# Performance work log

Hardware: AMD Instinct MI355X
Metric: run time of the kernel (lower is better)

The kernel has to match this reference:

```python
import jax, jax.numpy as jnp
import numpy as np
from jax import lax

B, S, D, H = 32, 1024, 1024, 1024


def setup_inputs() -> dict:
    key = jax.random.key(0)
    k_x, k_wx, k_wh, k_b = jax.random.split(key, 4)
    x = jax.random.normal(k_x, (B, S, D), dtype=jnp.float32)
    # Vanilla RNN cell parameters: h' = tanh(x @ Wx + h @ Wh + b)
    Wx = jax.random.normal(k_wx, (D, H), dtype=jnp.float32) / np.sqrt(D)
    Wh = jax.random.normal(k_wh, (H, H), dtype=jnp.float32) / np.sqrt(H)
    b = jnp.zeros((H,), dtype=jnp.float32)
    # initial_hidden weight, zero-initialized as in the keras layer
    h0 = jnp.zeros((H,), dtype=jnp.float32)
    return {"x": x, "Wx": Wx, "Wh": Wh, "b": b, "h0": h0}


def reference(x, Wx, Wh, b, h0):
    # x: [B, S, D] -> scan over time (seq-major, like tf.scan on transposed input)
    batch = x.shape[0]
    h_init = jnp.tile(h0[None, :], (batch, 1))  # [B, H]

    def step(h, x_t):
        h_new = jnp.tanh(x_t @ Wx + h @ Wh + b)  # [B, H]
        return h_new, h_new

    x_sbd = jnp.transpose(x, (1, 0, 2))  # [S, B, D]
    _, out_sbh = lax.scan(step, h_init, x_sbd)
    return jnp.transpose(out_sbh, (1, 0, 2))  # [B, S, H]
```

## Files before the change

kernel.cpp:

```cpp
#include <hip/hip_runtime.h>
#include <hip/hip_bf16.h>


#define BB 32
#define SS 1024
#define DD 1024
#define HH 1024
#define NG 32
#define BG 8
#define WGN (NG * BG)

#define CFENCE() asm volatile("" ::: "memory")

typedef unsigned long long ull;

__global__ __launch_bounds__(256) void xw_gemm(const float* __restrict__ A,
                                               const float* __restrict__ W,
                                               const float* __restrict__ bias,
                                               float* __restrict__ C) {
    __shared__ float As[8][132];
    __shared__ float Bs[8][132];
    const int tid = threadIdx.x;
    const int n0 = blockIdx.x * 128;
    const int m0 = blockIdx.y * 128;
    const int tx = tid & 15;
    const int ty = tid >> 4;
    const int ar = tid >> 1;
    const int ak = (tid & 1) * 4;
    const int bk = tid >> 5;
    const int bn = (tid & 31) * 4;

    float acc[8][8];
#pragma unroll
    for (int i = 0; i < 8; ++i)
#pragma unroll
        for (int j = 0; j < 8; ++j) acc[i][j] = 0.f;

    for (int k0 = 0; k0 < DD; k0 += 8) {
        float4 av = *(const float4*)(A + (size_t)(m0 + ar) * DD + k0 + ak);
        float4 bv = *(const float4*)(W + (size_t)(k0 + bk) * HH + n0 + bn);
        __syncthreads();
        As[ak + 0][ar] = av.x;
        As[ak + 1][ar] = av.y;
        As[ak + 2][ar] = av.z;
        As[ak + 3][ar] = av.w;
        *(float4*)&Bs[bk][bn] = bv;
        __syncthreads();
#pragma unroll
        for (int k = 0; k < 8; ++k) {
            float4 a0 = *(const float4*)&As[k][ty * 4];
            float4 a1 = *(const float4*)&As[k][64 + ty * 4];
            float4 b0 = *(const float4*)&Bs[k][tx * 4];
            float4 b1 = *(const float4*)&Bs[k][64 + tx * 4];
            float ar_[8] = {a0.x, a0.y, a0.z, a0.w, a1.x, a1.y, a1.z, a1.w};
            float br_[8] = {b0.x, b0.y, b0.z, b0.w, b1.x, b1.y, b1.z, b1.w};
#pragma unroll
            for (int i = 0; i < 8; ++i)
#pragma unroll
                for (int j = 0; j < 8; ++j)
                    acc[i][j] = fmaf(ar_[i], br_[j], acc[i][j]);
        }
    }

    float4 bv0 = *(const float4*)(bias + n0 + tx * 4);
    float4 bv1 = *(const float4*)(bias + n0 + 64 + tx * 4);
#pragma unroll
    for (int i = 0; i < 8; ++i) {
        int m = m0 + ((i < 4) ? (ty * 4 + i) : (64 + ty * 4 + (i - 4)));
        float4 r0 = {acc[i][0] + bv0.x, acc[i][1] + bv0.y,
                     acc[i][2] + bv0.z, acc[i][3] + bv0.w};
        float4 r1 = {acc[i][4] + bv1.x, acc[i][5] + bv1.y,
                     acc[i][6] + bv1.z, acc[i][7] + bv1.w};
        *(float4*)(C + (size_t)m * HH + n0 + tx * 4) = r0;
        *(float4*)(C + (size_t)m * HH + n0 + 64 + tx * 4) = r1;
    }
}

__global__ __launch_bounds__(256) void transpose_wh(const float* __restrict__ in,
                                                    float* __restrict__ outT) {
    __shared__ float tile[32][33];
    const int tx = threadIdx.x & 31;
    const int ty = threadIdx.x >> 5;
    const int x0 = blockIdx.x * 32;
    const int y0 = blockIdx.y * 32;
    for (int r = ty; r < 32; r += 8)
        tile[r][tx] = in[(size_t)(y0 + r) * HH + x0 + tx];
    __syncthreads();
    for (int r = ty; r < 32; r += 8)
        outT[(size_t)(x0 + r) * HH + y0 + tx] = tile[tx][r];
}

#define FMA_HALF(HALF)                                                         \
    {                                                                          \
        const int kb = (HALF) * 512 + kq * 4;                                  \
        float4 h[4];                                                           \
        _Pragma("unroll") for (int b = 0; b < 4; ++b)                          \
            h[b] = *(const float4*)&hs[b][kb];                                 \
        _Pragma("unroll") for (int b = 0; b < 4; ++b)                          \
            _Pragma("unroll") for (int c = 0; c < 16; ++c)                     \
                a[b * 16 + c] += h[b].x * wreg[HALF][c].x +                    \
                                 h[b].y * wreg[HALF][c].y +                    \
                                 h[b].z * wreg[HALF][c].z +                    \
                                 h[b].w * wreg[HALF][c].w;                     \
    }

__global__ __launch_bounds__(256, 1) void rnn_persist(
    const float* __restrict__ Wh, const float* __restrict__ WhT,
    const float* __restrict__ h0, float* __restrict__ out,
    unsigned int* __restrict__ flags, float* __restrict__ hbuf) {
    __shared__ float hs[4][1024];
    __shared__ float red[4][64];
    __shared__ float hout[4][32];

    const int tid  = threadIdx.x;
    const int ng   = blockIdx.x & 31;
    const int bg   = blockIdx.x >> 5;
    const int n0   = ng * 32;
    const int b0   = bg * 4;
    const int lane = tid & 63;
    const int wv   = tid >> 6;
    const int ns   = tid >> 7;
    const int kq   = tid & 127;
    unsigned int* cnt = flags + bg * 64;

    float4 wreg[2][16];
    if (WhT) {
        const float* base = WhT + (size_t)(n0 + ns * 16) * HH + kq * 4;
#pragma unroll
        for (int c = 0; c < 16; ++c) {
            wreg[0][c] = *(const float4*)(base + (size_t)c * HH);
            wreg[1][c] = *(const float4*)(base + (size_t)c * HH + 512);
        }
    } else {
#pragma unroll
        for (int c = 0; c < 16; ++c) {
            float v[8];
            for (int j = 0; j < 4; ++j)
                v[j] = Wh[(size_t)(kq * 4 + j) * HH + n0 + ns * 16 + c];
            for (int j = 0; j < 4; ++j)
                v[4 + j] = Wh[(size_t)(512 + kq * 4 + j) * HH + n0 + ns * 16 + c];
            wreg[0][c] = {v[0], v[1], v[2], v[3]};
            wreg[1][c] = {v[4], v[5], v[6], v[7]};
        }
    }

    size_t xp_base = 0;
    int eb = 0, ec = 0;
    if (tid < 128) {
        int l   = tid & 63;
        int idx = (int)(__brev((unsigned)l) >> 26);
        eb = idx >> 4;
        ec = (tid >> 6) * 16 + (idx & 15);
        xp_base = ((size_t)(b0 + eb) * SS) * HH + (n0 + ec);
    }

    for (int t = 0; t < SS; ++t) {
        float xp = 0.f;
        if (tid < 128) xp = out[xp_base + (size_t)t * HH];

        float a[64];
#pragma unroll
        for (int i = 0; i < 64; ++i) a[i] = 0.f;

        if (t == 0) {
#pragma unroll
            for (int j = 0; j < 4; ++j) {
                int f4 = tid + 256 * j;
                int r = f4 >> 8, c4 = (f4 & 255) * 4;
                *(float4*)&hs[r][c4] = *(const float4*)(h0 + c4);
            }
            __syncthreads();
            FMA_HALF(0)
            FMA_HALF(1)
        } else {
            if (tid == 0) {
                const unsigned target = (unsigned)t * 32u;
                while (__hip_atomic_load(cnt, __ATOMIC_RELAXED,
                                         __HIP_MEMORY_SCOPE_AGENT) < target) {
                }
            }
            CFENCE();
            __syncthreads();
            CFENCE();

            const ull* hsrc = (const ull*)(hbuf + (size_t)((t - 1) & 1) * BB * HH);
            ull hr[8];
#pragma unroll
            for (int j = 0; j < 4; ++j)
                hr[j] = __hip_atomic_load(hsrc + (size_t)(b0 + j) * 512 + tid,
                                          __ATOMIC_RELAXED, __HIP_MEMORY_SCOPE_AGENT);
#pragma unroll
            for (int j = 0; j < 4; ++j)
                hr[4 + j] = __hip_atomic_load(hsrc + (size_t)(b0 + j) * 512 + 256 + tid,
                                              __ATOMIC_RELAXED, __HIP_MEMORY_SCOPE_AGENT);
#pragma unroll
            for (int j = 0; j < 4; ++j)
                *(ull*)&hs[j][tid * 2] = hr[j];
            __syncthreads();
            FMA_HALF(0)
#pragma unroll
            for (int j = 0; j < 4; ++j)
                *(ull*)&hs[j][512 + tid * 2] = hr[4 + j];
            __syncthreads();
            FMA_HALF(1)
        }

        int s = 64;
#pragma unroll
        for (int m = 1; m <= 32; m <<= 1) {
            const int hs_ = s >> 1;
            const bool hi = (lane & m) != 0;
#pragma unroll
            for (int i = 0; i < hs_; ++i) {
                float lo = a[i], hg = a[i + hs_];
                a[i]       = hi ? hg : lo;
                a[i + hs_] = hi ? lo : hg;
            }
#pragma unroll
            for (int i = 0; i < hs_; ++i) a[i] += __shfl_xor(a[i + hs_], m, 64);
            s = hs_;
        }

        red[wv][lane] = a[0];
        __syncthreads();

        if (tid < 128) {
            const int l = tid & 63;
            const int nss = tid >> 6;
            float v = red[nss * 2][l] + red[nss * 2 + 1][l];
            float hv = tanhf(v + xp);
            out[xp_base + (size_t)t * HH] = hv;
            hout[eb][ec] = hv;
        }
        __syncthreads();

        if (tid < 64) {
            const int r  = tid >> 4;
            const int c2 = tid & 15;
            ull u = *(const ull*)&hout[r][c2 * 2];
            ull old = __hip_atomic_exchange(
                (ull*)(hbuf + (size_t)(t & 1) * BB * HH) +
                    (size_t)(b0 + r) * 512 + (n0 >> 1) + c2,
                u, __ATOMIC_RELAXED, __HIP_MEMORY_SCOPE_AGENT);
            asm volatile("" ::"v"(old));
        }

        CFENCE();
        __syncthreads();
        CFENCE();
        if (tid == 0)
            __hip_atomic_fetch_add(cnt, 1u, __ATOMIC_RELAXED,
                                   __HIP_MEMORY_SCOPE_AGENT);
    }
}

__global__ __launch_bounds__(256) void h0wh(const float* __restrict__ Wh,
                                            const float* __restrict__ h0,
                                            float* __restrict__ c) {
    const int g = blockIdx.x;
    const int n = threadIdx.x * 4;
    float4 a = {0.f, 0.f, 0.f, 0.f};
    for (int kk = 0; kk < 16; ++kk) {
        int k = g * 16 + kk;
        float hv = h0[k];
        float4 w = *(const float4*)(Wh + (size_t)k * HH + n);
        a.x += hv * w.x; a.y += hv * w.y; a.z += hv * w.z; a.w += hv * w.w;
    }
    atomicAdd(&c[n + 0], a.x);
    atomicAdd(&c[n + 1], a.y);
    atomicAdd(&c[n + 2], a.z);
    atomicAdd(&c[n + 3], a.w);
}

__global__ __launch_bounds__(256) void t0_kernel(float* __restrict__ out,
                                                 const float* __restrict__ c) {
    const int idx = blockIdx.x * 256 + threadIdx.x;
    const int b = idx >> 10;
    const int n = idx & 1023;
    const size_t p = (size_t)b * SS * HH + n;
    out[p] = tanhf(out[p] + c[n]);
}

__global__ __launch_bounds__(256) void rnn_step(const float* __restrict__ Wh,
                                                float* __restrict__ out, int t) {
    __shared__ float hsl[8][1028];
    __shared__ float ps[256];
    const int tid = threadIdx.x;
    const int n0 = blockIdx.x * 16;
    const int b0 = blockIdx.y * 8;
    for (int i = tid; i < 8 * 256; i += 256) {
        int r = i >> 8;
        int c = (i & 255) << 2;
        *(float4*)&hsl[r][c] =
            *(const float4*)(out + ((size_t)(b0 + r) * SS + (t - 1)) * HH + c);
    }
    __syncthreads();
    const int nl = tid & 15;
    const int bl = (tid >> 4) & 7;
    const int half_ = tid >> 7;
    const int n = n0 + nl;
    float acc = 0.f;
    const float* hrow = &hsl[bl][half_ * 512];
    const float* wcol = Wh + (size_t)(half_ * 512) * HH + n;
#pragma unroll 4
    for (int k = 0; k < 512; k += 4) {
        float4 h4 = *(const float4*)(hrow + k);
        acc += h4.x * wcol[(size_t)(k + 0) * HH];
        acc += h4.y * wcol[(size_t)(k + 1) * HH];
        acc += h4.z * wcol[(size_t)(k + 2) * HH];
        acc += h4.w * wcol[(size_t)(k + 3) * HH];
    }
    ps[tid] = acc;
    __syncthreads();
    if (tid < 128) {
        const size_t obase = ((size_t)(b0 + bl) * SS + t) * HH + n;
        out[obase] = tanhf(out[obase] + ps[tid] + ps[tid + 128]);
    }
}

extern "C" void kernel_launch(void* const* d_in, const int* in_sizes, int n_in,
                              void* d_out, int out_size, void* d_ws, size_t ws_size,
                              hipStream_t stream) {
    const float* x    = (const float*)d_in[0];
    const float* Wx   = (const float*)d_in[1];
    const float* Wh   = (const float*)d_in[2];
    const float* bias = (const float*)d_in[3];
    const float* h0   = (const float*)d_in[4];
    float* out = (float*)d_out;
    float* ws  = (float*)d_ws;

    xw_gemm<<<dim3(8, 256), 256, 0, stream>>>(x, Wx, bias, out);

    const size_t need_persist = (size_t)(512 + 2 * BB * HH) * sizeof(float);
    const size_t need_wht     = need_persist + (size_t)HH * HH * sizeof(float);

    if (ws_size >= need_persist) {
        unsigned int* flags = (unsigned int*)ws;
        float* hbuf = ws + 512;
        hipMemsetAsync(flags, 0, 2048, stream);

        const float* WhT = nullptr;
        if (ws_size >= need_wht) {
            float* whtp = ws + 512 + 2 * BB * HH;
            transpose_wh<<<dim3(32, 32), 256, 0, stream>>>(Wh, whtp);
            WhT = whtp;
        }

        void* kargs[] = {(void*)&Wh, (void*)&WhT, (void*)&h0, (void*)&out,
                         (void*)&flags, (void*)&hbuf};
        hipError_t rc = hipLaunchCooperativeKernel((const void*)rnn_persist,
                                                   dim3(WGN), dim3(256), kargs, 0,
                                                   stream);
        if (rc != hipSuccess) {
            rnn_persist<<<dim3(WGN), dim3(256), 0, stream>>>(Wh, WhT, h0, out,
                                                             flags, hbuf);
        }
    } else {
        float* cvec = ws;
        hipMemsetAsync(cvec, 0, HH * sizeof(float), stream);
        h0wh<<<64, 256, 0, stream>>>(Wh, h0, cvec);
        t0_kernel<<<BB * HH / 256, 256, 0, stream>>>(out, cvec);
        for (int t = 1; t < SS; ++t)
            rnn_step<<<dim3(64, 4), 256, 0, stream>>>(Wh, out, t);
    }
}
```

Before: 5.111 ms.

## Split each workgroup into two batch groups and overlap their recurrence steps

```diff
diff --git a/kernel.cpp b/kernel.cpp
--- a/kernel.cpp
+++ b/kernel.cpp
@@ -6,13 +6,14 @@
 #define SS 1024
 #define DD 1024
 #define HH 1024
-#define NG 32
-#define BG 8
-#define WGN (NG * BG)
+#define NPAIR 4
+#define WGN 256
 
 #define CFENCE() asm volatile("" ::: "memory")
 
 typedef unsigned long long ull;
+
+#define ALD(p) __hip_atomic_load((p), __ATOMIC_RELAXED, __HIP_MEMORY_SCOPE_AGENT)
 
 __global__ __launch_bounds__(256) void xw_gemm(const float* __restrict__ A,
                                                const float* __restrict__ W,
@@ -90,166 +91,222 @@
         outT[(size_t)(x0 + r) * HH + y0 + tx] = tile[tx][r];
 }
 
-#define FMA_HALF(HALF)                                                         \
+#define FMA4(HSB, ACC, HALF)                                                   \
     {                                                                          \
         const int kb = (HALF) * 512 + kq * 4;                                  \
-        float4 h[4];                                                           \
+        float4 h_[4];                                                          \
         _Pragma("unroll") for (int b = 0; b < 4; ++b)                          \
-            h[b] = *(const float4*)&hs[b][kb];                                 \
+            h_[b] = *(const float4*)&HSB[b][kb];                               \
         _Pragma("unroll") for (int b = 0; b < 4; ++b)                          \
-            _Pragma("unroll") for (int c = 0; c < 16; ++c)                     \
-                a[b * 16 + c] += h[b].x * wreg[HALF][c].x +                    \
-                                 h[b].y * wreg[HALF][c].y +                    \
-                                 h[b].z * wreg[HALF][c].z +                    \
-                                 h[b].w * wreg[HALF][c].w;                     \
+            _Pragma("unroll") for (int c = 0; c < 8; ++c)                      \
+                ACC[b * 8 + c] += h_[b].x * wreg[HALF][c].x +                  \
+                                  h_[b].y * wreg[HALF][c].y +                  \
+                                  h_[b].z * wreg[HALF][c].z +                  \
+                                  h_[b].w * wreg[HALF][c].w;                   \
+    }
+
+#define FOLD32(ACC)                                                            \
+    {                                                                          \
+        int s_ = 32;                                                           \
+        _Pragma("unroll") for (int m = 1; m <= 16; m <<= 1) {                  \
+            const int hh_ = s_ >> 1;                                           \
+            const bool hi = (lane & m) != 0;                                   \
+            _Pragma("unroll") for (int i = 0; i < hh_; ++i) {                  \
+                float lo = ACC[i], hg = ACC[i + hh_];                          \
+                ACC[i]       = hi ? hg : lo;                                   \
+                ACC[i + hh_] = hi ? lo : hg;                                   \
+            }                                                                  \
+            _Pragma("unroll") for (int i = 0; i < hh_; ++i)                    \
+                ACC[i] += __shfl_xor(ACC[i + hh_], m, 64);                     \
+            s_ = hh_;                                                          \
+        }                                                                      \
     }
 
 __global__ __launch_bounds__(256, 1) void rnn_persist(
     const float* __restrict__ Wh, const float* __restrict__ WhT,
     const float* __restrict__ h0, float* __restrict__ out,
     unsigned int* __restrict__ flags, float* __restrict__ hbuf) {
-    __shared__ float hs[4][1024];
+    __shared__ float hsA[4][1024];
+    __shared__ float hsB[4][1024];
     __shared__ float red[4][64];
-    __shared__ float hout[4][32];
+    __shared__ float houtA[4][16];
+    __shared__ float houtB[4][16];
 
     const int tid  = threadIdx.x;
-    const int ng   = blockIdx.x & 31;
-    const int bg   = blockIdx.x >> 5;
-    const int n0   = ng * 32;
-    const int b0   = bg * 4;
+    const int p    = blockIdx.x & 3;
+    const int ng   = blockIdx.x >> 2;
+    const int n0   = ng * 16;
+    const int b0A  = p * 8;
+    const int b0B  = p * 8 + 4;
     const int lane = tid & 63;
     const int wv   = tid >> 6;
     const int ns   = tid >> 7;
     const int kq   = tid & 127;
-    unsigned int* cnt = flags + bg * 64;
-
-    float4 wreg[2][16];
+    unsigned int* cntA = flags + (2 * p) * 64;
+    unsigned int* cntB = flags + (2 * p + 1) * 64;
+
+    float4 wreg[2][8];
     if (WhT) {
-        const float* base = WhT + (size_t)(n0 + ns * 16) * HH + kq * 4;
-#pragma unroll
-        for (int c = 0; c < 16; ++c) {
+        const float* base = WhT + (size_t)(n0 + ns * 8) * HH + kq * 4;
+#pragma unroll
+        for (int c = 0; c < 8; ++c) {
             wreg[0][c] = *(const float4*)(base + (size_t)c * HH);
             wreg[1][c] = *(const float4*)(base + (size_t)c * HH + 512);
         }
     } else {
 #pragma unroll
-        for (int c = 0; c < 16; ++c) {
+        for (int c = 0; c < 8; ++c) {
             float v[8];
             for (int j = 0; j < 4; ++j)
-                v[j] = Wh[(size_t)(kq * 4 + j) * HH + n0 + ns * 16 + c];
-            for (int j = 0; j < 4; ++j)
-                v[4 + j] = Wh[(size_t)(512 + kq * 4 + j) * HH + n0 + ns * 16 + c];
+                v[j] = Wh[(size_t)(kq * 4 + j) * HH + n0 + ns * 8 + c];
+            for (int j = 0; j < 4; ++j)
+                v[4 + j] = Wh[(size_t)(512 + kq * 4 + j) * HH + n0 + ns * 8 + c];
             wreg[0][c] = {v[0], v[1], v[2], v[3]};
             wreg[1][c] = {v[4], v[5], v[6], v[7]};
         }
     }
 
     size_t xp_base = 0;
-    int eb = 0, ec = 0;
+    int eb = 0, ec = 0, l5 = 0, nso = 0;
     if (tid < 128) {
-        int l   = tid & 63;
-        int idx = (int)(__brev((unsigned)l) >> 26);
-        eb = idx >> 4;
-        ec = (tid >> 6) * 16 + (idx & 15);
-        xp_base = ((size_t)(b0 + eb) * SS) * HH + (n0 + ec);
+        int ct = tid & 63;
+        nso = ct >> 5;
+        int o = ct & 31;
+        eb = o >> 3;
+        ec = nso * 8 + (o & 7);
+        l5 = (int)(__brev((unsigned)o) >> 27);
+        int myb0 = (tid < 64) ? b0A : b0B;
+        xp_base = ((size_t)(myb0 + eb) * SS) * HH + (n0 + ec);
     }
 
     for (int t = 0; t < SS; ++t) {
         float xp = 0.f;
         if (tid < 128) xp = out[xp_base + (size_t)t * HH];
 
-        float a[64];
-#pragma unroll
-        for (int i = 0; i < 64; ++i) a[i] = 0.f;
+        ull hrB[8];
+        const ull* hsrc = (const ull*)(hbuf + (size_t)((t - 1) & 1) * BB * HH);
 
         if (t == 0) {
+            int c4 = tid * 4;
+            float4 v = *(const float4*)(h0 + c4);
 #pragma unroll
             for (int j = 0; j < 4; ++j) {
-                int f4 = tid + 256 * j;
-                int r = f4 >> 8, c4 = (f4 & 255) * 4;
-                *(float4*)&hs[r][c4] = *(const float4*)(h0 + c4);
+                *(float4*)&hsA[j][c4] = v;
+                *(float4*)&hsB[j][c4] = v;
             }
             __syncthreads();
-            FMA_HALF(0)
-            FMA_HALF(1)
         } else {
             if (tid == 0) {
-                const unsigned target = (unsigned)t * 32u;
-                while (__hip_atomic_load(cnt, __ATOMIC_RELAXED,
-                                         __HIP_MEMORY_SCOPE_AGENT) < target) {
+                const unsigned target = (unsigned)t * 64u;
+                while (ALD(cntA) < target) {
                 }
             }
             CFENCE();
             __syncthreads();
             CFENCE();
-
-            const ull* hsrc = (const ull*)(hbuf + (size_t)((t - 1) & 1) * BB * HH);
-            ull hr[8];
-#pragma unroll
-            for (int j = 0; j < 4; ++j)
-                hr[j] = __hip_atomic_load(hsrc + (size_t)(b0 + j) * 512 + tid,
-                                          __ATOMIC_RELAXED, __HIP_MEMORY_SCOPE_AGENT);
-#pragma unroll
-            for (int j = 0; j < 4; ++j)
-                hr[4 + j] = __hip_atomic_load(hsrc + (size_t)(b0 + j) * 512 + 256 + tid,
-                                              __ATOMIC_RELAXED, __HIP_MEMORY_SCOPE_AGENT);
-#pragma unroll
-            for (int j = 0; j < 4; ++j)
-                *(ull*)&hs[j][tid * 2] = hr[j];
+            ull hrA[8];
+#pragma unroll
+            for (int j = 0; j < 4; ++j)
+                hrA[j] = ALD(hsrc + (size_t)(b0A + j) * 512 + tid);
+#pragma unroll
+            for (int j = 0; j < 4; ++j)
+                hrA[4 + j] = ALD(hsrc + (size_t)(b0A + j) * 512 + 256 + tid);
+            if (tid == 0) {
+                const unsigned target = (unsigned)t * 64u;
+                while (ALD(cntB) < target) {
+                }
+            }
+#pragma unroll
+            for (int j = 0; j < 4; ++j) {
+                *(ull*)&hsA[j][tid * 2] = hrA[j];
+                *(ull*)&hsA[j][512 + tid * 2] = hrA[4 + j];
+            }
+            CFENCE();
             __syncthreads();
-            FMA_HALF(0)
-#pragma unroll
-            for (int j = 0; j < 4; ++j)
-                *(ull*)&hs[j][512 + tid * 2] = hr[4 + j];
-            __syncthreads();
-            FMA_HALF(1)
-        }
-
-        int s = 64;
-#pragma unroll
-        for (int m = 1; m <= 32; m <<= 1) {
-            const int hs_ = s >> 1;
-            const bool hi = (lane & m) != 0;
-#pragma unroll
-            for (int i = 0; i < hs_; ++i) {
-                float lo = a[i], hg = a[i + hs_];
-                a[i]       = hi ? hg : lo;
-                a[i + hs_] = hi ? lo : hg;
-            }
-#pragma unroll
-            for (int i = 0; i < hs_; ++i) a[i] += __shfl_xor(a[i + hs_], m, 64);
-            s = hs_;
-        }
-
-        red[wv][lane] = a[0];
-        __syncthreads();
-
-        if (tid < 128) {
-            const int l = tid & 63;
-            const int nss = tid >> 6;
-            float v = red[nss * 2][l] + red[nss * 2 + 1][l];
+            CFENCE();
+#pragma unroll
+            for (int j = 0; j < 4; ++j)
+                hrB[j] = ALD(hsrc + (size_t)(b0B + j) * 512 + tid);
+#pragma unroll
+            for (int j = 0; j < 4; ++j)
+                hrB[4 + j] = ALD(hsrc + (size_t)(b0B + j) * 512 + 256 + tid);
+        }
+
+        float aA[32];
+#pragma unroll
+        for (int i = 0; i < 32; ++i) aA[i] = 0.f;
+        FMA4(hsA, aA, 0)
+        FMA4(hsA, aA, 1)
+        FOLD32(aA)
+        red[wv][lane] = aA[0];
+        __syncthreads();
+
+        if (tid < 64) {
+            float v = red[2 * nso][l5] + red[2 * nso][l5 + 32] +
+                      red[2 * nso + 1][l5] + red[2 * nso + 1][l5 + 32];
             float hv = tanhf(v + xp);
             out[xp_base + (size_t)t * HH] = hv;
-            hout[eb][ec] = hv;
-        }
-        __syncthreads();
-
-        if (tid < 64) {
-            const int r  = tid >> 4;
-            const int c2 = tid & 15;
-            ull u = *(const ull*)&hout[r][c2 * 2];
-            ull old = __hip_atomic_exchange(
-                (ull*)(hbuf + (size_t)(t & 1) * BB * HH) +
-                    (size_t)(b0 + r) * 512 + (n0 >> 1) + c2,
-                u, __ATOMIC_RELAXED, __HIP_MEMORY_SCOPE_AGENT);
+            houtA[eb][ec] = hv;
+        }
+        __syncthreads();
+
+        if (tid < 32) {
+            const int r  = tid >> 3;
+            const int c2 = tid & 7;
+            ull u = *(const ull*)&houtA[r][c2 * 2];
+            ull* ptr = (ull*)(hbuf + (size_t)(t & 1) * BB * HH) +
+                       (size_t)(b0A + r) * 512 + ng * 8 + c2;
+            ull old = __hip_atomic_exchange(ptr, u, __ATOMIC_RELAXED,
+                                            __HIP_MEMORY_SCOPE_AGENT);
             asm volatile("" ::"v"(old));
         }
-
+        if (t > 0) {
+#pragma unroll
+            for (int j = 0; j < 4; ++j) {
+                *(ull*)&hsB[j][tid * 2] = hrB[j];
+                *(ull*)&hsB[j][512 + tid * 2] = hrB[4 + j];
+            }
+        }
         CFENCE();
         __syncthreads();
         CFENCE();
         if (tid == 0)
-            __hip_atomic_fetch_add(cnt, 1u, __ATOMIC_RELAXED,
+            __hip_atomic_fetch_add(cntA, 1u, __ATOMIC_RELAXED,
+                                   __HIP_MEMORY_SCOPE_AGENT);
+
+        float aB[32];
+#pragma unroll
+        for (int i = 0; i < 32; ++i) aB[i] = 0.f;
+        FMA4(hsB, aB, 0)
+        FMA4(hsB, aB, 1)
+        FOLD32(aB)
+        red[wv][lane] = aB[0];
+        __syncthreads();
+
+        if (tid >= 64 && tid < 128) {
+            float v = red[2 * nso][l5] + red[2 * nso][l5 + 32] +
+                      red[2 * nso + 1][l5] + red[2 * nso + 1][l5 + 32];
+            float hv = tanhf(v + xp);
+            out[xp_base + (size_t)t * HH] = hv;
+            houtB[eb][ec] = hv;
+        }
+        __syncthreads();
+
+        if (tid < 32) {
+            const int r  = tid >> 3;
+            const int c2 = tid & 7;
+            ull u = *(const ull*)&houtB[r][c2 * 2];
+            ull* ptr = (ull*)(hbuf + (size_t)(t & 1) * BB * HH) +
+                       (size_t)(b0B + r) * 512 + ng * 8 + c2;
+            ull old = __hip_atomic_exchange(ptr, u, __ATOMIC_RELAXED,
+                                            __HIP_MEMORY_SCOPE_AGENT);
+            asm volatile("" ::"v"(old));
+        }
+        CFENCE();
+        __syncthreads();
+        CFENCE();
+        if (tid == 0)
+            __hip_atomic_fetch_add(cntB, 1u, __ATOMIC_RELAXED,
                                    __HIP_MEMORY_SCOPE_AGENT);
     }
 }
```

Result: slower. 6.112 ms (+19.6%).

## Replace counter barrier with parity-tagged hidden-state data polling

Applied to the files above, without the earlier changes.

```diff
diff --git a/kernel.cpp b/kernel.cpp
--- a/kernel.cpp
+++ b/kernel.cpp
@@ -10,9 +10,9 @@
 #define BG 8
 #define WGN (NG * BG)
 
-#define CFENCE() asm volatile("" ::: "memory")
-
 typedef unsigned long long ull;
+
+#define ALD(p) __hip_atomic_load((p), __ATOMIC_RELAXED, __HIP_MEMORY_SCOPE_AGENT)
 
 __global__ __launch_bounds__(256) void xw_gemm(const float* __restrict__ A,
                                                const float* __restrict__ W,
@@ -107,7 +107,7 @@
 __global__ __launch_bounds__(256, 1) void rnn_persist(
     const float* __restrict__ Wh, const float* __restrict__ WhT,
     const float* __restrict__ h0, float* __restrict__ out,
-    unsigned int* __restrict__ flags, float* __restrict__ hbuf) {
+    float* __restrict__ hbuf) {
     __shared__ float hs[4][1024];
     __shared__ float red[4][64];
     __shared__ float hout[4][32];
@@ -121,7 +121,8 @@
     const int wv   = tid >> 6;
     const int ns   = tid >> 7;
     const int kq   = tid & 127;
-    unsigned int* cnt = flags + bg * 64;
+
+    const ull TAGMASK = ~((1ull << 30) | (1ull << 62));
 
     float4 wreg[2][16];
     if (WhT) {
@@ -173,35 +174,31 @@
             FMA_HALF(0)
             FMA_HALF(1)
         } else {
-            if (tid == 0) {
-                const unsigned target = (unsigned)t * 32u;
-                while (__hip_atomic_load(cnt, __ATOMIC_RELAXED,
-                                         __HIP_MEMORY_SCOPE_AGENT) < target) {
+            const ull* hsrc = (const ull*)hbuf + (size_t)((t - 1) & 1) * BB * 512;
+            const unsigned pc = ((unsigned)(t - 1) >> 1) & 1u;
+            ull w[8];
+            for (;;) {
+#pragma unroll
+                for (int j = 0; j < 4; ++j)
+                    w[j] = ALD(hsrc + (size_t)(b0 + j) * 512 + tid);
+#pragma unroll
+                for (int j = 0; j < 4; ++j)
+                    w[4 + j] = ALD(hsrc + (size_t)(b0 + j) * 512 + 256 + tid);
+                unsigned bad = 0;
+#pragma unroll
+                for (int j = 0; j < 8; ++j) {
+                    bad |= (((unsigned)(w[j] >> 30)) ^ pc) & 1u;
+                    bad |= (((unsigned)(w[j] >> 62)) ^ pc) & 1u;
                 }
+                if (!bad) break;
             }
-            CFENCE();
-            __syncthreads();
-            CFENCE();
-
-            const ull* hsrc = (const ull*)(hbuf + (size_t)((t - 1) & 1) * BB * HH);
-            ull hr[8];
-#pragma unroll
-            for (int j = 0; j < 4; ++j)
-                hr[j] = __hip_atomic_load(hsrc + (size_t)(b0 + j) * 512 + tid,
-                                          __ATOMIC_RELAXED, __HIP_MEMORY_SCOPE_AGENT);
-#pragma unroll
-            for (int j = 0; j < 4; ++j)
-                hr[4 + j] = __hip_atomic_load(hsrc + (size_t)(b0 + j) * 512 + 256 + tid,
-                                              __ATOMIC_RELAXED, __HIP_MEMORY_SCOPE_AGENT);
-#pragma unroll
-            for (int j = 0; j < 4; ++j)
-                *(ull*)&hs[j][tid * 2] = hr[j];
+#pragma unroll
+            for (int j = 0; j < 4; ++j) {
+                *(ull*)&hs[j][tid * 2] = w[j] & TAGMASK;
+                *(ull*)&hs[j][512 + tid * 2] = w[4 + j] & TAGMASK;
+            }
             __syncthreads();
             FMA_HALF(0)
-#pragma unroll
-            for (int j = 0; j < 4; ++j)
-                *(ull*)&hs[j][512 + tid * 2] = hr[4 + j];
-            __syncthreads();
             FMA_HALF(1)
         }
 
@@ -237,20 +234,14 @@
         if (tid < 64) {
             const int r  = tid >> 4;
             const int c2 = tid & 15;
+            const ull pp = (ull)(((unsigned)t >> 1) & 1u);
             ull u = *(const ull*)&hout[r][c2 * 2];
-            ull old = __hip_atomic_exchange(
-                (ull*)(hbuf + (size_t)(t & 1) * BB * HH) +
+            u |= (pp << 30) | (pp << 62);
+            __hip_atomic_store(
+                (ull*)hbuf + (size_t)(t & 1) * BB * 512 +
                     (size_t)(b0 + r) * 512 + (n0 >> 1) + c2,
                 u, __ATOMIC_RELAXED, __HIP_MEMORY_SCOPE_AGENT);
-            asm volatile("" ::"v"(old));
-        }
-
-        CFENCE();
-        __syncthreads();
-        CFENCE();
-        if (tid == 0)
-            __hip_atomic_fetch_add(cnt, 1u, __ATOMIC_RELAXED,
-                                   __HIP_MEMORY_SCOPE_AGENT);
+        }
     }
 }
 
@@ -331,29 +322,28 @@
 
     xw_gemm<<<dim3(8, 256), 256, 0, stream>>>(x, Wx, bias, out);
 
-    const size_t need_persist = (size_t)(512 + 2 * BB * HH) * sizeof(float);
+    const size_t need_persist = (size_t)(2 * BB * HH) * sizeof(float);
     const size_t need_wht     = need_persist + (size_t)HH * HH * sizeof(float);
 
     if (ws_size >= need_persist) {
-        unsigned int* flags = (unsigned int*)ws;
-        float* hbuf = ws + 512;
-        hipMemsetAsync(flags, 0, 2048, stream);
+        float* hbuf = ws;
+        hipMemsetAsync(hbuf, 0xFF, need_persist, stream);
 
         const float* WhT = nullptr;
         if (ws_size >= need_wht) {
-            float* whtp = ws + 512 + 2 * BB * HH;
+            float* whtp = ws + 2 * BB * HH;
             transpose_wh<<<dim3(32, 32), 256, 0, stream>>>(Wh, whtp);
             WhT = whtp;
         }
 
         void* kargs[] = {(void*)&Wh, (void*)&WhT, (void*)&h0, (void*)&out,
-                         (void*)&flags, (void*)&hbuf};
+                         (void*)&hbuf};
         hipError_t rc = hipLaunchCooperativeKernel((const void*)rnn_persist,
                                                    dim3(WGN), dim3(256), kargs, 0,
                                                    stream);
         if (rc != hipSuccess) {
             rnn_persist<<<dim3(WGN), dim3(256), 0, stream>>>(Wh, WhT, h0, out,
-                                                             flags, hbuf);
+                                                             hbuf);
         }
     } else {
         float* cvec = ws;
```

New measurement: 4.859 ms, median of 2. 4.9% less time.
